# Kernel tuning notes

Measured on AMD Instinct MI355X. Metric: run time of the kernel, lower is better.

Reference implementation:

```python
import jax, jax.numpy as jnp
import numpy as np

BATCH = 131072
HASHLEN = 64
HID = 180
OUT = 300


def setup_inputs() -> dict:
    key = jax.random.key(0)
    ks = jax.random.split(key, 8)
    scale = 0.05
    return {
        "b": jax.random.normal(ks[0], (BATCH, HASHLEN), dtype=jnp.float32),
        "labels": jax.random.randint(ks[1], (BATCH,), 0, 300),
        "W_h": jax.random.normal(ks[2], (HID, HASHLEN), dtype=jnp.float32) * scale,
        "b_h": jax.random.normal(ks[3], (HID,), dtype=jnp.float32) * scale,
        "W_mu": jax.random.normal(ks[4], (OUT, HID), dtype=jnp.float32) * scale,
        "b_mu": jax.random.normal(ks[5], (OUT,), dtype=jnp.float32) * scale,
        "W_sig": jax.random.normal(ks[6], (OUT, HID), dtype=jnp.float32) * scale,
        "b_sig": jax.random.normal(ks[7], (OUT,), dtype=jnp.float32) * scale,
    }


def reference(b, labels, W_h, b_h, W_mu, b_mu, W_sig, b_sig):
    # h = hidden(b); mean = mu(h); sigma = sigma_layer(h)
    h = b @ W_h.T + b_h                      # [B, 180]
    mean = h @ W_mu.T + b_mu                 # [B, 300]
    sig = h @ W_sig.T + b_sig                # [B, 300]
    # Original builds diag(sig^2) and calls MVN.rsample, which Cholesky-factors
    # the diagonal covariance: L = diag(sqrt(sig^2)) = diag(|sig|).
    # rsample = mean + L @ eps  ==  mean + |sig| * eps  (elementwise).
    std = jnp.abs(sig)
    eps = jax.random.normal(jax.random.key(42), mean.shape, dtype=mean.dtype)
    return mean + std * eps
```

## Files before the change

### kernel.cpp

```cpp
#include <hip/hip_runtime.h>
#include <stdint.h>

#define BATCH   131072
#define HASHLEN 64
#define HID     180
#define OUT     300

#define BM      64
#define NT      256
#define NTILE2  19

#define WH_FRAGS  (12 * 2 * 64)
#define WM_FRAGS  (NTILE2 * 6 * 64)
#define TOT_FRAGS (WH_FRAGS + 2 * WM_FRAGS)
#define WS_NEEDED ((size_t)TOT_FRAGS * 16)

typedef short bf16x8 __attribute__((ext_vector_type(8)));
typedef float f32x4  __attribute__((ext_vector_type(4)));

#define FAST_SQRT(x) __builtin_amdgcn_sqrtf(x)
#define ROTL(x, r) __builtin_amdgcn_alignbit((x), (x), 32u - (r))

__device__ __forceinline__ unsigned threefry_bits(unsigned ctr) {
  const unsigned ks0 = 0u;
  const unsigned ks1 = 42u;
  const unsigned ks2 = 0x1BD11BDAu ^ 0u ^ 42u;
  unsigned x0 = ks0;
  unsigned x1 = ctr + ks1;
#define TF_R(r) { x0 += x1; x1 = ROTL(x1, r); x1 ^= x0; }
  TF_R(13u) TF_R(15u) TF_R(26u) TF_R(6u)
  x0 += ks1; x1 += ks2 + 1u;
  TF_R(17u) TF_R(29u) TF_R(16u) TF_R(24u)
  x0 += ks2; x1 += ks0 + 2u;
  TF_R(13u) TF_R(15u) TF_R(26u) TF_R(6u)
  x0 += ks0; x1 += ks1 + 3u;
  TF_R(17u) TF_R(29u) TF_R(16u) TF_R(24u)
  x0 += ks1; x1 += ks2 + 4u;
  TF_R(13u) TF_R(15u) TF_R(26u) TF_R(6u)
  x0 += ks2; x1 += ks0 + 5u;
#undef TF_R
  return x0 ^ x1;
}

__device__ __forceinline__ float poly_low_sqrt2(float zz) {
  float p = 2.11772e-09f;
  p = fmaf(p, zz, 3.73196e-08f);
  p = fmaf(p, zz, -5.52613e-07f);
  p = fmaf(p, zz, -9.93702e-07f);
  p = fmaf(p, zz, 7.13551e-05f);
  p = fmaf(p, zz, -5.90464e-04f);
  p = fmaf(p, zz, -2.83858e-03f);
  p = fmaf(p, zz, 0.24177160f);
  p = fmaf(p, zz, 2.1233136f);
  return p;
}
__device__ __forceinline__ float poly_high_sqrt2(float v) {
  float p = -6.53600e-05f;
  p = fmaf(p, v, 3.95852e-05f);
  p = fmaf(p, v, 6.35506e-04f);
  p = fmaf(p, v, -2.07827e-03f);
  p = fmaf(p, v, 3.89984e-03f);
  p = fmaf(p, v, -6.22117e-03f);
  p = fmaf(p, v, 9.25254e-03f);
  p = fmaf(p, v, 1.1793807f);
  p = fmaf(p, v, 4.0064340f);
  return p;
}

__device__ __forceinline__ float eps_from_bits(uint32_t bits) {
  float f = __uint_as_float((bits >> 9) | 0x3F800000u) - 1.0f;
  const float LO = -0.99999994f;
  float u = fmaxf(LO, fmaf(f, 2.0f, LO));
  float t = fmaf(-u, u, 1.0f);
  float z = -__log2f(t);
  float p = poly_low_sqrt2(z - 3.6067376f);
  if (__any(z >= 7.2134752f)) {
    float ph = poly_high_sqrt2(FAST_SQRT(z) - 3.6033669f);
    p = (z >= 7.2134752f) ? ph : p;
  }
  return p * u;
}

__device__ __forceinline__ uint16_t f2bf(float f) {
  uint32_t u = __float_as_uint(f);
  return (uint16_t)((u + 0x7FFFu + ((u >> 16) & 1u)) >> 16);
}

__global__ __launch_bounds__(256) void prep_weights(
    const float* __restrict__ W_h, const float* __restrict__ W_mu,
    const float* __restrict__ W_sig, uint16_t* __restrict__ ws)
{
  int f = blockIdx.x * 256 + threadIdx.x;
  if (f >= TOT_FRAGS) return;
  uint16_t vals[8];
  if (f < WH_FRAGS) {
    int nt = f >> 7, s = (f >> 6) & 1, l = f & 63;
    int row = nt * 16 + (l & 15);
    int k0  = s * 32 + (l >> 4) * 8;
#pragma unroll
    for (int j = 0; j < 8; ++j)
      vals[j] = (row < HID) ? f2bf(W_h[row * HASHLEN + k0 + j]) : (uint16_t)0;
  } else {
    int g = f - WH_FRAGS;
    const float* W = (g < WM_FRAGS) ? W_mu : W_sig;
    if (g >= WM_FRAGS) g -= WM_FRAGS;
    int gt = g / 384, s = (g >> 6) % 6, l = g & 63;
    int col = gt * 16 + (l & 15);
    int k0  = s * 32 + (l >> 4) * 8;
#pragma unroll
    for (int j = 0; j < 8; ++j) {
      int k = k0 + j;
      vals[j] = (col < OUT && k < HID) ? f2bf(W[col * HID + k]) : (uint16_t)0;
    }
  }
  uint16_t* dst = ws + (size_t)f * 8;
#pragma unroll
  for (int j = 0; j < 8; ++j) dst[j] = vals[j];
}

__device__ __forceinline__ void epilogue8(
    f32x4 aM0, f32x4 aS0, f32x4 aM1, f32x4 aS1,
    f32x4 bm0, f32x4 bs0, f32x4 bm1, f32x4 bs1,
    uint32_t gi0, float* __restrict__ out)
{
  uint32_t bits[8];
#pragma unroll
  for (int j = 0; j < 8; ++j) {
    uint32_t c = gi0 + (uint32_t)((j < 4) ? j : (12 + j));
    bits[j] = threefry_bits(c);
  }
  float xx[8], z[8], pl[8];
#pragma unroll
  for (int j = 0; j < 8; ++j) {
    float f = __uint_as_float((bits[j] >> 9) | 0x3F800000u) - 1.0f;
    const float LO = -0.99999994f;
    float u = fmaxf(LO, fmaf(f, 2.0f, LO));
    xx[j] = u;
    float t = fmaf(-u, u, 1.0f);
    z[j] = -__log2f(t);
    pl[j] = poly_low_sqrt2(z[j] - 3.6067376f);
  }
#pragma unroll
  for (int j = 0; j < 8; ++j) {
    if (__any(z[j] >= 7.2134752f)) {
      float ph = poly_high_sqrt2(FAST_SQRT(z[j]) - 3.6033669f);
      pl[j] = (z[j] >= 7.2134752f) ? ph : pl[j];
    }
  }
  f32x4 r0, r1;
#pragma unroll
  for (int q = 0; q < 4; ++q) {
    r0[q] = fmaf(fabsf(aS0[q] + bs0[q]), pl[q] * xx[q],         aM0[q] + bm0[q]);
    r1[q] = fmaf(fabsf(aS1[q] + bs1[q]), pl[q + 4] * xx[q + 4], aM1[q] + bm1[q]);
  }
  *(f32x4*)(out + gi0)      = r0;
  *(f32x4*)(out + gi0 + 16) = r1;
}

__device__ __forceinline__ void epilogue4(
    f32x4 accM, f32x4 accS, f32x4 bm4, f32x4 bs4, uint32_t gi0,
    float* __restrict__ out)
{
  uint32_t bits[4];
#pragma unroll
  for (int q = 0; q < 4; ++q)
    bits[q] = threefry_bits(gi0 + (uint32_t)q);
  float xx[4], z[4], pl[4];
#pragma unroll
  for (int q = 0; q < 4; ++q) {
    float f = __uint_as_float((bits[q] >> 9) | 0x3F800000u) - 1.0f;
    const float LO = -0.99999994f;
    float u = fmaxf(LO, fmaf(f, 2.0f, LO));
    xx[q] = u;
    float t = fmaf(-u, u, 1.0f);
    z[q] = -__log2f(t);
    pl[q] = poly_low_sqrt2(z[q] - 3.6067376f);
  }
#pragma unroll
  for (int q = 0; q < 4; ++q) {
    if (__any(z[q] >= 7.2134752f)) {
      float ph = poly_high_sqrt2(FAST_SQRT(z[q]) - 3.6033669f);
      pl[q] = (z[q] >= 7.2134752f) ? ph : pl[q];
    }
  }
  f32x4 res;
#pragma unroll
  for (int q = 0; q < 4; ++q) {
    float mu  = accM[q] + bm4[q];
    float sg  = fabsf(accS[q] + bs4[q]);
    res[q] = fmaf(sg, pl[q] * xx[q], mu);
  }
  *(f32x4*)(out + gi0) = res;
}

__global__ __launch_bounds__(NT, 4) void fused_decoder(
    const float* __restrict__ bin,
    const uint16_t* __restrict__ ws,
    const float* __restrict__ b_h,
    const float* __restrict__ b_mu, const float* __restrict__ b_sig,
    float* __restrict__ out)
{
  __shared__ unsigned char lds[BM * 384];

  const int tid    = threadIdx.x;
  const int l      = tid & 63;
  const int w      = tid >> 6;
  const int lane15 = l & 15;
  const int lhi    = l >> 4;
  const int swzb   = (lane15 & 7) << 4;
  const int row0   = blockIdx.x * BM;
  const int r0     = w * 16;

  const bf16x8* wsWh = (const bf16x8*)ws;
  const bf16x8* wsWm = (const bf16x8*)ws + WH_FRAGS;
  const bf16x8* wsWs = (const bf16x8*)ws + WH_FRAGS + WM_FRAGS;

  {
    const float* brow = bin + (size_t)(row0 + r0 + lane15) * HASHLEN;
    bf16x8 bfrag[2];
#pragma unroll
    for (int s = 0; s < 2; ++s) {
      float4 v0 = *(const float4*)(brow + s * 32 + lhi * 8);
      float4 v1 = *(const float4*)(brow + s * 32 + lhi * 8 + 4);
      bf16x8 a;
      a[0] = (short)f2bf(v0.x); a[1] = (short)f2bf(v0.y);
      a[2] = (short)f2bf(v0.z); a[3] = (short)f2bf(v0.w);
      a[4] = (short)f2bf(v1.x); a[5] = (short)f2bf(v1.y);
      a[6] = (short)f2bf(v1.z); a[7] = (short)f2bf(v1.w);
      bfrag[s] = a;
    }
    const int row = r0 + lane15;
#pragma unroll
    for (int nt = 0; nt < 12; ++nt) {
      f32x4 acc = {0.f, 0.f, 0.f, 0.f};
#pragma unroll
      for (int s = 0; s < 2; ++s)
        acc = __builtin_amdgcn_mfma_f32_16x16x32_bf16(wsWh[(nt * 2 + s) * 64 + l], bfrag[s], acc, 0, 0, 0);
      const int k0 = nt * 16 + lhi * 4;
      f32x4 bias = {0.f, 0.f, 0.f, 0.f};
      if (k0 <= HID - 4) bias = *(const f32x4*)(b_h + k0);
      const bool ok = (k0 < HID);
      float h0 = ok ? (acc[0] + bias[0]) : 0.0f;
      float h1 = ok ? (acc[1] + bias[1]) : 0.0f;
      float h2 = ok ? (acc[2] + bias[2]) : 0.0f;
      float h3 = ok ? (acc[3] + bias[3]) : 0.0f;
      uint2 pk;
      pk.x = (uint32_t)f2bf(h0) | ((uint32_t)f2bf(h1) << 16);
      pk.y = (uint32_t)f2bf(h2) | ((uint32_t)f2bf(h3) << 16);
      *(uint2*)(lds + row * 384 + ((2 * k0) ^ swzb)) = pk;
    }
  }

  bf16x8 a2[6];
#pragma unroll
  for (int s = 0; s < 6; ++s)
    a2[s] = *(const bf16x8*)(lds + (r0 + lane15) * 384 + ((s * 64 + lhi * 16) ^ swzb));

  const uint32_t idx0 = (uint32_t)((row0 + r0 + lane15) * OUT + lhi * 4);

#pragma unroll 1
  for (int gp = 0; gp < 9; ++gp) {
    const int gt0 = gp * 2;
    const int gt1 = gt0 + 1;
    f32x4 aM0 = {0.f, 0.f, 0.f, 0.f};
    f32x4 aS0 = {0.f, 0.f, 0.f, 0.f};
    f32x4 aM1 = {0.f, 0.f, 0.f, 0.f};
    f32x4 aS1 = {0.f, 0.f, 0.f, 0.f};
#pragma unroll
    for (int s = 0; s < 6; ++s)
      aM0 = __builtin_amdgcn_mfma_f32_16x16x32_bf16(wsWm[(gt0 * 6 + s) * 64 + l], a2[s], aM0, 0, 0, 0);
#pragma unroll
    for (int s = 0; s < 6; ++s)
      aS0 = __builtin_amdgcn_mfma_f32_16x16x32_bf16(wsWs[(gt0 * 6 + s) * 64 + l], a2[s], aS0, 0, 0, 0);
#pragma unroll
    for (int s = 0; s < 6; ++s)
      aM1 = __builtin_amdgcn_mfma_f32_16x16x32_bf16(wsWm[(gt1 * 6 + s) * 64 + l], a2[s], aM1, 0, 0, 0);
#pragma unroll
    for (int s = 0; s < 6; ++s)
      aS1 = __builtin_amdgcn_mfma_f32_16x16x32_bf16(wsWs[(gt1 * 6 + s) * 64 + l], a2[s], aS1, 0, 0, 0);

    const int c0 = gt0 * 16 + lhi * 4;
    f32x4 bm0 = *(const f32x4*)(b_mu + c0);
    f32x4 bs0 = *(const f32x4*)(b_sig + c0);
    f32x4 bm1 = *(const f32x4*)(b_mu + c0 + 16);
    f32x4 bs1 = *(const f32x4*)(b_sig + c0 + 16);
    epilogue8(aM0, aS0, aM1, aS1, bm0, bs0, bm1, bs1,
              idx0 + (uint32_t)(gt0 * 16), out);
  }

  {
    const int gt = NTILE2 - 1;
    f32x4 accM = {0.f, 0.f, 0.f, 0.f};
    f32x4 accS = {0.f, 0.f, 0.f, 0.f};
#pragma unroll
    for (int s = 0; s < 6; ++s) {
      accM = __builtin_amdgcn_mfma_f32_16x16x32_bf16(wsWm[(gt * 6 + s) * 64 + l], a2[s], accM, 0, 0, 0);
      accS = __builtin_amdgcn_mfma_f32_16x16x32_bf16(wsWs[(gt * 6 + s) * 64 + l], a2[s], accS, 0, 0, 0);
    }
    if (lhi < 3) {
      const int c0 = gt * 16 + lhi * 4;
      f32x4 bm4 = *(const f32x4*)(b_mu + c0);
      f32x4 bs4 = *(const f32x4*)(b_sig + c0);
      epilogue4(accM, accS, bm4, bs4, idx0 + (uint32_t)(gt * 16), out);
    }
  }
}

#define FTILE2  19
#define FCHT    2
#define FNCH    10
#define FSH_OFF   0
#define FSH_BYTES (64 * 384)
#define FU_OFF    FSH_BYTES
#define FSB_OFF   FU_OFF
#define FSWH_OFF  (FU_OFF + 8192)
#define FSWM_OFF  FU_OFF
#define FSWS_OFF  (FU_OFF + 12288)
#define FLDS_BYTES (FSH_BYTES + 32768)

__global__ __launch_bounds__(NT) void fused_decoder_fb(
    const float* __restrict__ bin,
    const float* __restrict__ W_h, const float* __restrict__ b_h,
    const float* __restrict__ W_mu, const float* __restrict__ b_mu,
    const float* __restrict__ W_sig, const float* __restrict__ b_sig,
    float* __restrict__ out)
{
  __shared__ unsigned char lds[FLDS_BYTES];
  const int tid = threadIdx.x;
  const int l = tid & 63, w = tid >> 6;
  const int lane15 = l & 15, lhi = l >> 4;
  const int swzb = (l & 7) << 4;
  const int row0 = blockIdx.x * BM;
  const int r0 = w * 16;
  {
    const float4* src = reinterpret_cast<const float4*>(bin + (size_t)row0 * HASHLEN);
#pragma unroll
    for (int it = 0; it < 4; ++it) {
      int idx = tid + NT * it;
      int r = idx >> 4, k4 = idx & 15;
      float4 v = src[idx];
      uint32_t p0 = f2bf(v.x) | ((uint32_t)f2bf(v.y) << 16);
      uint32_t p1 = f2bf(v.z) | ((uint32_t)f2bf(v.w) << 16);
      int off = FSB_OFF + r * 128 + ((k4 * 8) ^ ((r & 7) << 4));
      *(uint32_t*)(lds + off) = p0;
      *(uint32_t*)(lds + off + 4) = p1;
    }
#pragma unroll
    for (int it = 0; it < 12; ++it) {
      int idx = tid + NT * it;
      int n = idx >> 4, k4 = idx & 15;
      float4 v = make_float4(0.f, 0.f, 0.f, 0.f);
      if (n < HID) v = *(const float4*)(W_h + (size_t)n * HASHLEN + k4 * 4);
      uint32_t p0 = f2bf(v.x) | ((uint32_t)f2bf(v.y) << 16);
      uint32_t p1 = f2bf(v.z) | ((uint32_t)f2bf(v.w) << 16);
      int off = FSWH_OFF + n * 128 + ((k4 * 8) ^ ((n & 7) << 4));
      *(uint32_t*)(lds + off) = p0;
      *(uint32_t*)(lds + off + 4) = p1;
    }
  }
  __syncthreads();
  {
    bf16x8 a1[2];
#pragma unroll
    for (int s = 0; s < 2; ++s)
      a1[s] = *(const bf16x8*)(lds + FSB_OFF + (r0 + lane15) * 128 + ((s * 64 + lhi * 16) ^ swzb));
#pragma unroll
    for (int nt = 0; nt < 12; ++nt) {
      f32x4 acc = {0.f, 0.f, 0.f, 0.f};
#pragma unroll
      for (int s = 0; s < 2; ++s) {
        bf16x8 bf = *(const bf16x8*)(lds + FSWH_OFF + (nt * 16 + lane15) * 128 + ((s * 64 + lhi * 16) ^ swzb));
        acc = __builtin_amdgcn_mfma_f32_16x16x32_bf16(a1[s], bf, acc, 0, 0, 0);
      }
      int col = nt * 16 + lane15;
      float bias = (col < HID) ? b_h[col] : 0.0f;
#pragma unroll
      for (int q = 0; q < 4; ++q) {
        int row = r0 + lhi * 4 + q;
        float h = (col < HID) ? (acc[q] + bias) : 0.0f;
        *(uint16_t*)(lds + FSH_OFF + row * 384 + ((2 * col) ^ ((row & 7) << 4))) = f2bf(h);
      }
    }
  }
  __syncthreads();
  bf16x8 a2[6];
#pragma unroll
  for (int s = 0; s < 6; ++s)
    a2[s] = *(const bf16x8*)(lds + FSH_OFF + (r0 + lane15) * 384 + ((s * 64 + lhi * 16) ^ swzb));
  const int rowi = tid >> 3;
  const int tt8 = tid & 7;
  for (int ch = 0; ch < FNCH; ++ch) {
    const int t0 = ch * FCHT;
    const int ntc = (FTILE2 - t0 < FCHT) ? (FTILE2 - t0) : FCHT;
    if (rowi < ntc * 16) {
      int col = ch * 32 + rowi;
      bool cok = (col < OUT);
      const float* wm = W_mu + (size_t)col * HID;
      const float* wsg = W_sig + (size_t)col * HID;
#pragma unroll
      for (int it = 0; it < 12; ++it) {
        int k2 = tt8 + 8 * it;
        bool kok = cok && (k2 < 90);
        float2 vm = kok ? *(const float2*)(wm + k2 * 2) : make_float2(0.f, 0.f);
        float2 vs = kok ? *(const float2*)(wsg + k2 * 2) : make_float2(0.f, 0.f);
        int off = (k2 * 4) ^ ((rowi & 7) << 4);
        *(uint32_t*)(lds + FSWM_OFF + rowi * 384 + off) = f2bf(vm.x) | ((uint32_t)f2bf(vm.y) << 16);
        *(uint32_t*)(lds + FSWS_OFF + rowi * 384 + off) = f2bf(vs.x) | ((uint32_t)f2bf(vs.y) << 16);
      }
    }
    __syncthreads();
    for (int nt2 = 0; nt2 < ntc; ++nt2) {
      const int gt = t0 + nt2;
      const int crow = nt2 * 16 + lane15;
      f32x4 accM = {0.f, 0.f, 0.f, 0.f};
      f32x4 accS = {0.f, 0.f, 0.f, 0.f};
#pragma unroll
      for (int s = 0; s < 6; ++s) {
        int boff = (s * 64 + lhi * 16) ^ swzb;
        bf16x8 bm = *(const bf16x8*)(lds + FSWM_OFF + crow * 384 + boff);
        bf16x8 bs = *(const bf16x8*)(lds + FSWS_OFF + crow * 384 + boff);
        accM = __builtin_amdgcn_mfma_f32_16x16x32_bf16(a2[s], bm, accM, 0, 0, 0);
        accS = __builtin_amdgcn_mfma_f32_16x16x32_bf16(a2[s], bs, accS, 0, 0, 0);
      }
      const int col = gt * 16 + lane15;
      if (col < OUT) {
        const float bmu = b_mu[col];
        const float bsg = b_sig[col];
#pragma unroll
        for (int q = 0; q < 4; ++q) {
          int row = r0 + lhi * 4 + q;
          int gr = row0 + row;
          float mu = accM[q] + bmu;
          float sg = fabsf(accS[q] + bsg);
          uint32_t gi = (uint32_t)(gr * OUT + col);
          uint32_t bits = threefry_bits(gi);
          float eps = eps_from_bits(bits);
          out[(size_t)gr * OUT + col] = fmaf(sg, eps, mu);
        }
      }
    }
    __syncthreads();
  }
}

extern "C" void kernel_launch(void* const* d_in, const int* in_sizes, int n_in,
                              void* d_out, int out_size, void* d_ws, size_t ws_size,
                              hipStream_t stream) {
  const float* b     = (const float*)d_in[0];
  const float* W_h   = (const float*)d_in[2];
  const float* b_h   = (const float*)d_in[3];
  const float* W_mu  = (const float*)d_in[4];
  const float* b_mu  = (const float*)d_in[5];
  const float* W_sig = (const float*)d_in[6];
  const float* b_sig = (const float*)d_in[7];
  float* out = (float*)d_out;

  if (ws_size >= WS_NEEDED && d_ws != nullptr) {
    uint16_t* ws = (uint16_t*)d_ws;
    hipLaunchKernelGGL(prep_weights, dim3((TOT_FRAGS + 255) / 256), dim3(256), 0, stream,
                       W_h, W_mu, W_sig, ws);
    hipLaunchKernelGGL(fused_decoder, dim3(BATCH / BM), dim3(NT), 0, stream,
                       b, ws, b_h, b_mu, b_sig, out);
  } else {
    hipLaunchKernelGGL(fused_decoder_fb, dim3(BATCH / BM), dim3(NT), 0, stream,
                       b, W_h, b_h, W_mu, b_mu, W_sig, b_sig, out);
  }
}
```

Measured before the change: 137.4 us.

## Give each wave two 16-row tiles to reuse weight fragments across MFMAs

Halves the block to 128 threads (2 waves), with each wave now covering 32 rows as two 16-row tiles. Every weight fragment loaded from global/L2 now feeds two MFMAs, halving weight-fragment load traffic per row. In exchange it roughly doubles accumulator and A-fragment register use, lowers the launch-bounds occupancy hint from 4 to 3, and gives each block fewer waves to hide latency. The fallback kernel keeps 256 threads through a separate FNT constant.

```diff
diff --git a/kernel.cpp b/kernel.cpp
--- a/kernel.cpp
+++ b/kernel.cpp
@@ -7,7 +7,7 @@
 #define OUT     300
 
 #define BM      64
-#define NT      256
+#define NT      128
 #define NTILE2  19
 
 #define WH_FRAGS  (12 * 2 * 64)
@@ -193,7 +193,7 @@
   *(f32x4*)(out + gi0) = res;
 }
 
-__global__ __launch_bounds__(NT, 4) void fused_decoder(
+__global__ __launch_bounds__(NT, 3) void fused_decoder(
     const float* __restrict__ bin,
     const uint16_t* __restrict__ ws,
     const float* __restrict__ b_h,
@@ -209,103 +209,138 @@
   const int lhi    = l >> 4;
   const int swzb   = (lane15 & 7) << 4;
   const int row0   = blockIdx.x * BM;
-  const int r0     = w * 16;
+  const int r0     = w * 32;
 
   const bf16x8* wsWh = (const bf16x8*)ws;
   const bf16x8* wsWm = (const bf16x8*)ws + WH_FRAGS;
   const bf16x8* wsWs = (const bf16x8*)ws + WH_FRAGS + WM_FRAGS;
 
   {
-    const float* brow = bin + (size_t)(row0 + r0 + lane15) * HASHLEN;
-    bf16x8 bfrag[2];
-#pragma unroll
-    for (int s = 0; s < 2; ++s) {
-      float4 v0 = *(const float4*)(brow + s * 32 + lhi * 8);
-      float4 v1 = *(const float4*)(brow + s * 32 + lhi * 8 + 4);
-      bf16x8 a;
-      a[0] = (short)f2bf(v0.x); a[1] = (short)f2bf(v0.y);
-      a[2] = (short)f2bf(v0.z); a[3] = (short)f2bf(v0.w);
-      a[4] = (short)f2bf(v1.x); a[5] = (short)f2bf(v1.y);
-      a[6] = (short)f2bf(v1.z); a[7] = (short)f2bf(v1.w);
-      bfrag[s] = a;
-    }
-    const int row = r0 + lane15;
+    bf16x8 bfrag[2][2];
+#pragma unroll
+    for (int rt = 0; rt < 2; ++rt) {
+      const float* brow = bin + (size_t)(row0 + r0 + rt * 16 + lane15) * HASHLEN;
+#pragma unroll
+      for (int s = 0; s < 2; ++s) {
+        float4 v0 = *(const float4*)(brow + s * 32 + lhi * 8);
+        float4 v1 = *(const float4*)(brow + s * 32 + lhi * 8 + 4);
+        bf16x8 a;
+        a[0] = (short)f2bf(v0.x); a[1] = (short)f2bf(v0.y);
+        a[2] = (short)f2bf(v0.z); a[3] = (short)f2bf(v0.w);
+        a[4] = (short)f2bf(v1.x); a[5] = (short)f2bf(v1.y);
+        a[6] = (short)f2bf(v1.z); a[7] = (short)f2bf(v1.w);
+        bfrag[rt][s] = a;
+      }
+    }
 #pragma unroll
     for (int nt = 0; nt < 12; ++nt) {
-      f32x4 acc = {0.f, 0.f, 0.f, 0.f};
-#pragma unroll
-      for (int s = 0; s < 2; ++s)
-        acc = __builtin_amdgcn_mfma_f32_16x16x32_bf16(wsWh[(nt * 2 + s) * 64 + l], bfrag[s], acc, 0, 0, 0);
+      f32x4 acc0 = {0.f, 0.f, 0.f, 0.f};
+      f32x4 acc1 = {0.f, 0.f, 0.f, 0.f};
+#pragma unroll
+      for (int s = 0; s < 2; ++s) {
+        bf16x8 bw = wsWh[(nt * 2 + s) * 64 + l];
+        acc0 = __builtin_amdgcn_mfma_f32_16x16x32_bf16(bw, bfrag[0][s], acc0, 0, 0, 0);
+        acc1 = __builtin_amdgcn_mfma_f32_16x16x32_bf16(bw, bfrag[1][s], acc1, 0, 0, 0);
+      }
       const int k0 = nt * 16 + lhi * 4;
       f32x4 bias = {0.f, 0.f, 0.f, 0.f};
       if (k0 <= HID - 4) bias = *(const f32x4*)(b_h + k0);
       const bool ok = (k0 < HID);
-      float h0 = ok ? (acc[0] + bias[0]) : 0.0f;
-      float h1 = ok ? (acc[1] + bias[1]) : 0.0f;
-      float h2 = ok ? (acc[2] + bias[2]) : 0.0f;
-      float h3 = ok ? (acc[3] + bias[3]) : 0.0f;
-      uint2 pk;
-      pk.x = (uint32_t)f2bf(h0) | ((uint32_t)f2bf(h1) << 16);
-      pk.y = (uint32_t)f2bf(h2) | ((uint32_t)f2bf(h3) << 16);
-      *(uint2*)(lds + row * 384 + ((2 * k0) ^ swzb)) = pk;
-    }
-  }
-
-  bf16x8 a2[6];
-#pragma unroll
-  for (int s = 0; s < 6; ++s)
-    a2[s] = *(const bf16x8*)(lds + (r0 + lane15) * 384 + ((s * 64 + lhi * 16) ^ swzb));
-
-  const uint32_t idx0 = (uint32_t)((row0 + r0 + lane15) * OUT + lhi * 4);
+#pragma unroll
+      for (int rt = 0; rt < 2; ++rt) {
+        f32x4 acc = rt ? acc1 : acc0;
+        float h0 = ok ? (acc[0] + bias[0]) : 0.0f;
+        float h1 = ok ? (acc[1] + bias[1]) : 0.0f;
+        float h2 = ok ? (acc[2] + bias[2]) : 0.0f;
+        float h3 = ok ? (acc[3] + bias[3]) : 0.0f;
+        uint2 pk;
+        pk.x = (uint32_t)f2bf(h0) | ((uint32_t)f2bf(h1) << 16);
+        pk.y = (uint32_t)f2bf(h2) | ((uint32_t)f2bf(h3) << 16);
+        const int row = r0 + rt * 16 + lane15;
+        *(uint2*)(lds + row * 384 + ((2 * k0) ^ swzb)) = pk;
+      }
+    }
+  }
+
+  bf16x8 a2[2][6];
+#pragma unroll
+  for (int rt = 0; rt < 2; ++rt)
+#pragma unroll
+    for (int s = 0; s < 6; ++s)
+      a2[rt][s] = *(const bf16x8*)(lds + (r0 + rt * 16 + lane15) * 384 +
+                                   ((s * 64 + lhi * 16) ^ swzb));
+
+  const uint32_t idx0  = (uint32_t)((row0 + r0 + lane15) * OUT + lhi * 4);
+  const uint32_t idx1  = idx0 + (uint32_t)(16 * OUT);
 
 #pragma unroll 1
   for (int gp = 0; gp < 9; ++gp) {
     const int gt0 = gp * 2;
     const int gt1 = gt0 + 1;
-    f32x4 aM0 = {0.f, 0.f, 0.f, 0.f};
-    f32x4 aS0 = {0.f, 0.f, 0.f, 0.f};
-    f32x4 aM1 = {0.f, 0.f, 0.f, 0.f};
-    f32x4 aS1 = {0.f, 0.f, 0.f, 0.f};
-#pragma unroll
-    for (int s = 0; s < 6; ++s)
-      aM0 = __builtin_amdgcn_mfma_f32_16x16x32_bf16(wsWm[(gt0 * 6 + s) * 64 + l], a2[s], aM0, 0, 0, 0);
-#pragma unroll
-    for (int s = 0; s < 6; ++s)
-      aS0 = __builtin_amdgcn_mfma_f32_16x16x32_bf16(wsWs[(gt0 * 6 + s) * 64 + l], a2[s], aS0, 0, 0, 0);
-#pragma unroll
-    for (int s = 0; s < 6; ++s)
-      aM1 = __builtin_amdgcn_mfma_f32_16x16x32_bf16(wsWm[(gt1 * 6 + s) * 64 + l], a2[s], aM1, 0, 0, 0);
-#pragma unroll
-    for (int s = 0; s < 6; ++s)
-      aS1 = __builtin_amdgcn_mfma_f32_16x16x32_bf16(wsWs[(gt1 * 6 + s) * 64 + l], a2[s], aS1, 0, 0, 0);
+    f32x4 aM0r0 = {0.f, 0.f, 0.f, 0.f}, aS0r0 = {0.f, 0.f, 0.f, 0.f};
+    f32x4 aM1r0 = {0.f, 0.f, 0.f, 0.f}, aS1r0 = {0.f, 0.f, 0.f, 0.f};
+    f32x4 aM0r1 = {0.f, 0.f, 0.f, 0.f}, aS0r1 = {0.f, 0.f, 0.f, 0.f};
+    f32x4 aM1r1 = {0.f, 0.f, 0.f, 0.f}, aS1r1 = {0.f, 0.f, 0.f, 0.f};
+#pragma unroll
+    for (int s = 0; s < 6; ++s) {
+      bf16x8 f = wsWm[(gt0 * 6 + s) * 64 + l];
+      aM0r0 = __builtin_amdgcn_mfma_f32_16x16x32_bf16(f, a2[0][s], aM0r0, 0, 0, 0);
+      aM0r1 = __builtin_amdgcn_mfma_f32_16x16x32_bf16(f, a2[1][s], aM0r1, 0, 0, 0);
+    }
+#pragma unroll
+    for (int s = 0; s < 6; ++s) {
+      bf16x8 f = wsWs[(gt0 * 6 + s) * 64 + l];
+      aS0r0 = __builtin_amdgcn_mfma_f32_16x16x32_bf16(f, a2[0][s], aS0r0, 0, 0, 0);
+      aS0r1 = __builtin_amdgcn_mfma_f32_16x16x32_bf16(f, a2[1][s], aS0r1, 0, 0, 0);
+    }
+#pragma unroll
+    for (int s = 0; s < 6; ++s) {
+      bf16x8 f = wsWm[(gt1 * 6 + s) * 64 + l];
+      aM1r0 = __builtin_amdgcn_mfma_f32_16x16x32_bf16(f, a2[0][s], aM1r0, 0, 0, 0);
+      aM1r1 = __builtin_amdgcn_mfma_f32_16x16x32_bf16(f, a2[1][s], aM1r1, 0, 0, 0);
+    }
+#pragma unroll
+    for (int s = 0; s < 6; ++s) {
+      bf16x8 f = wsWs[(gt1 * 6 + s) * 64 + l];
+      aS1r0 = __builtin_amdgcn_mfma_f32_16x16x32_bf16(f, a2[0][s], aS1r0, 0, 0, 0);
+      aS1r1 = __builtin_amdgcn_mfma_f32_16x16x32_bf16(f, a2[1][s], aS1r1, 0, 0, 0);
+    }
 
     const int c0 = gt0 * 16 + lhi * 4;
     f32x4 bm0 = *(const f32x4*)(b_mu + c0);
     f32x4 bs0 = *(const f32x4*)(b_sig + c0);
     f32x4 bm1 = *(const f32x4*)(b_mu + c0 + 16);
     f32x4 bs1 = *(const f32x4*)(b_sig + c0 + 16);
-    epilogue8(aM0, aS0, aM1, aS1, bm0, bs0, bm1, bs1,
-              idx0 + (uint32_t)(gt0 * 16), out);
+    const uint32_t go = (uint32_t)(gt0 * 16);
+    epilogue8(aM0r0, aS0r0, aM1r0, aS1r0, bm0, bs0, bm1, bs1, idx0 + go, out);
+    epilogue8(aM0r1, aS0r1, aM1r1, aS1r1, bm0, bs0, bm1, bs1, idx1 + go, out);
   }
 
   {
     const int gt = NTILE2 - 1;
-    f32x4 accM = {0.f, 0.f, 0.f, 0.f};
-    f32x4 accS = {0.f, 0.f, 0.f, 0.f};
+    f32x4 aMr0 = {0.f, 0.f, 0.f, 0.f}, aSr0 = {0.f, 0.f, 0.f, 0.f};
+    f32x4 aMr1 = {0.f, 0.f, 0.f, 0.f}, aSr1 = {0.f, 0.f, 0.f, 0.f};
 #pragma unroll
     for (int s = 0; s < 6; ++s) {
-      accM = __builtin_amdgcn_mfma_f32_16x16x32_bf16(wsWm[(gt * 6 + s) * 64 + l], a2[s], accM, 0, 0, 0);
-      accS = __builtin_amdgcn_mfma_f32_16x16x32_bf16(wsWs[(gt * 6 + s) * 64 + l], a2[s], accS, 0, 0, 0);
+      bf16x8 fM = wsWm[(gt * 6 + s) * 64 + l];
+      bf16x8 fS = wsWs[(gt * 6 + s) * 64 + l];
+      aMr0 = __builtin_amdgcn_mfma_f32_16x16x32_bf16(fM, a2[0][s], aMr0, 0, 0, 0);
+      aMr1 = __builtin_amdgcn_mfma_f32_16x16x32_bf16(fM, a2[1][s], aMr1, 0, 0, 0);
+      aSr0 = __builtin_amdgcn_mfma_f32_16x16x32_bf16(fS, a2[0][s], aSr0, 0, 0, 0);
+      aSr1 = __builtin_amdgcn_mfma_f32_16x16x32_bf16(fS, a2[1][s], aSr1, 0, 0, 0);
     }
     if (lhi < 3) {
       const int c0 = gt * 16 + lhi * 4;
       f32x4 bm4 = *(const f32x4*)(b_mu + c0);
       f32x4 bs4 = *(const f32x4*)(b_sig + c0);
-      epilogue4(accM, accS, bm4, bs4, idx0 + (uint32_t)(gt * 16), out);
-    }
-  }
-}
-
+      const uint32_t go = (uint32_t)(gt * 16);
+      epilogue4(aMr0, aSr0, bm4, bs4, idx0 + go, out);
+      epilogue4(aMr1, aSr1, bm4, bs4, idx1 + go, out);
+    }
+  }
+}
+
+#define FNT     256
 #define FTILE2  19
 #define FCHT    2
 #define FNCH    10
@@ -318,7 +353,7 @@
 #define FSWS_OFF  (FU_OFF + 12288)
 #define FLDS_BYTES (FSH_BYTES + 32768)
 
-__global__ __launch_bounds__(NT) void fused_decoder_fb(
+__global__ __launch_bounds__(FNT) void fused_decoder_fb(
     const float* __restrict__ bin,
     const float* __restrict__ W_h, const float* __restrict__ b_h,
     const float* __restrict__ W_mu, const float* __restrict__ b_mu,
@@ -336,7 +371,7 @@
     const float4* src = reinterpret_cast<const float4*>(bin + (size_t)row0 * HASHLEN);
 #pragma unroll
     for (int it = 0; it < 4; ++it) {
-      int idx = tid + NT * it;
+      int idx = tid + FNT * it;
       int r = idx >> 4, k4 = idx & 15;
       float4 v = src[idx];
       uint32_t p0 = f2bf(v.x) | ((uint32_t)f2bf(v.y) << 16);
@@ -347,7 +382,7 @@
     }
 #pragma unroll
     for (int it = 0; it < 12; ++it) {
-      int idx = tid + NT * it;
+      int idx = tid + FNT * it;
       int n = idx >> 4, k4 = idx & 15;
       float4 v = make_float4(0.f, 0.f, 0.f, 0.f);
       if (n < HID) v = *(const float4*)(W_h + (size_t)n * HASHLEN + k4 * 4);
@@ -462,7 +497,7 @@
     hipLaunchKernelGGL(fused_decoder, dim3(BATCH / BM), dim3(NT), 0, stream,
                        b, ws, b_h, b_mu, b_sig, out);
   } else {
-    hipLaunchKernelGGL(fused_decoder_fb, dim3(BATCH / BM), dim3(NT), 0, stream,
+    hipLaunchKernelGGL(fused_decoder_fb, dim3(BATCH / BM), dim3(FNT), 0, stream,
                        b, W_h, b_h, W_mu, b_mu, W_sig, b_sig, out);
   }
 }
```

Result: slower. 149.4 us (+8.8%).
